# Kernel tuning notes

Measured on AMD Instinct MI355X. Metric: run time of the kernel, lower is better.

Reference implementation:

```python
import jax, jax.numpy as jnp
import numpy as np
import jax.scipy.linalg as jsl

# ---- module constants (mirror __init__ buffers) ----
T0, T1, DT = 0.0, 1.0, 1e-3
DIM, NSTEPS, M, TQ, B = 8, 2048, 64, 1024, 1
DS = (T1 - T0) / NSTEPS
STEPS = jnp.linspace(T0, T1, NSTEPS + 1)            # [S+1]
ZPTS = jnp.linspace(T0 + DT * 5.5, T1 - DT * 5.5, M)  # inducing points [M]
SQRT_DS = float(np.sqrt(DS))
SQRT_DT = float(np.sqrt(DT))


def _hurst(t, y0, W1, b1, W2, b2, Wc1, bc1, Wc2, bc2, dw, cw):
    # compute_hurst: sigmoid(driving_action(t)*dw + condition_net(y0)*cw)
    tc_in = t.reshape(-1, 1)                                             # [N,1]
    feat = jnp.concatenate([jnp.sin(tc_in), jnp.cos(tc_in), tc_in], -1)  # [N,3]
    tc = jax.nn.sigmoid(jnp.tanh(feat @ W1.T + b1) @ W2.T + b2)          # [N,dim]
    pc = jax.nn.sigmoid(jnp.tanh(y0 @ Wc1.T + bc1) @ Wc2.T + bc2)        # [1,dim]
    return jax.nn.sigmoid(tc * dw + pc * cw)                             # [N,dim]


def _safe_pow(x, a):
    # x**a for x>=0, with well-defined (zero) gradient at x==0
    mask = x > 0
    xs = jnp.where(mask, x, 1.0)
    return jnp.where(mask, xs ** a, 0.0)


def _compute_weight(t, y0, params, eps=1e-12):
    # compute_weight (Muniandy et al. weight); returns [S, N, dim]
    h = _hurst(t, y0, *params)[None]                              # [1,N,dim]
    d0 = jax.nn.relu(t[None, :] - STEPS[:-1, None])[..., None]    # [S,N,1]
    d1 = jax.nn.relu(t[None, :] - STEPS[1:, None])[..., None]     # [S,N,1]
    w = jnp.sqrt(_safe_pow(d0, 2.0 * h) - _safe_pow(d1, 2.0 * h) + eps)
    w = w / jnp.sqrt(2.0 * h * DS)
    return w / jnp.exp(jax.lax.lgamma(h + 0.5))


def _increment_weight(t, y0, params):
    # increment_weight: g_i / dt (finite difference of clamped weights)
    wa = jnp.maximum(_compute_weight(t, y0, params), 0.0)
    wb = jnp.maximum(_compute_weight(t + DT, y0, params), 0.0)
    return jnp.maximum((wb - wa) * SQRT_DS / DT, 0.0)             # [S,N,dim]


def _forward(t, y0, eps_z, W1, b1, W2, b2, Wc1, bc1, Wc2, bc2, dw, cw):
    params = (W1, b1, W2, b2, Wc1, bc1, Wc2, bc2, dw, cw)
    # --- precompute (inducing points) ---
    Kz = _increment_weight(ZPTS, y0, params)                # [S,M,dim]
    Kzz = jnp.einsum('smd,skd->dmk', Kz, Kz)                # [dim,M,M]
    Lz = jnp.linalg.cholesky(Kzz + 1e-6 * jnp.eye(M, dtype=Kzz.dtype))
    delta_Bz = jnp.einsum('dmk,dkb->dmb', Lz, eps_z)        # [dim,M,B]
    # --- forward (mean / sqrt(var)*sqrt(dt)) ---
    Kt = _increment_weight(t, y0, params)                   # [S,T,dim]
    Ktz = jnp.einsum('std,smd->dtm', Kt, Kz)                # [dim,T,M]
    alpha = jax.vmap(lambda L, b: jsl.cho_solve((L, True), b))(
        Lz, jnp.swapaxes(Ktz, -1, -2))                      # [dim,M,T]
    mean = jnp.einsum('dmt,dmb->dtb', alpha, delta_Bz)      # [dim,T,B]
    Ktt = jnp.einsum('std,sud->dtu', Kt, Kt)                # [dim,T,T]
    var = Ktt - jnp.einsum('dmt,dmu->dtu', alpha, alpha)    # [dim,T,T]
    std = jnp.sqrt(jnp.maximum(var, 1e-12)) * SQRT_DT
    return mean.reshape(-1, DIM), std.reshape(-1, DIM)


def setup_inputs() -> dict:
    key = jax.random.key(0)
    ks = jax.random.split(key, 12)
    return {
        't': jax.random.uniform(ks[0], (TQ,), jnp.float32, T0 + 0.05, T1 - 0.05),
        'y0': jax.random.normal(ks[1], (1, 1), jnp.float32),
        'eps_z': jax.random.normal(ks[2], (DIM, M, B), jnp.float32),
        'W1': jax.random.normal(ks[3], (10, 3), jnp.float32) * 0.3,
        'b1': jax.random.normal(ks[4], (10,), jnp.float32) * 0.1,
        'W2': jax.random.normal(ks[5], (DIM, 10), jnp.float32) * 0.3,
        'b2': jax.random.normal(ks[6], (DIM,), jnp.float32) * 0.1,
        'Wc1': jax.random.normal(ks[7], (10, 1), jnp.float32) * 0.3,
        'bc1': jax.random.normal(ks[8], (10,), jnp.float32) * 0.1,
        'Wc2': jax.random.normal(ks[9], (DIM, 10), jnp.float32) * 0.3,
        'bc2': jax.random.normal(ks[10], (DIM,), jnp.float32) * 0.1,
        'dw': jnp.array([0.5], jnp.float32),
        'cw': jnp.array([0.5], jnp.float32),
    }


def reference(t, y0, eps_z, W1, b1, W2, b2, Wc1, bc1, Wc2, bc2, dw, cw):
    return _forward(t, y0, eps_z, W1, b1, W2, b2, Wc1, bc1, Wc2, bc2, dw, cw)
```

## Files before the change

### kernel.cpp

```cpp
#include <hip/hip_runtime.h>
#include <cmath>

#define DIMN 8
#define SSTEPS 2048
#define MZ 64
#define TQN 1024
#define DS_F    4.8828125e-4f
#define DT_F    1.0e-3f
#define SCALE_F 22.09708691207961f
#define SQRTDT_F 0.031622776601683794f
#define LN2_F   0.6931471805599453f

typedef _Float16 f16x8 __attribute__((ext_vector_type(8)));
typedef float f32x4 __attribute__((ext_vector_type(4)));

__device__ __forceinline__ float sigmoidf_(float x) { return 1.f / (1.f + expf(-x)); }

__device__ __forceinline__ void gl_lds16(const _Float16* g, _Float16* l)
{
    __builtin_amdgcn_global_load_lds(
        (const __attribute__((address_space(1))) unsigned int*)g,
        (__attribute__((address_space(3))) unsigned int*)l, 16, 0, 0);
}

__global__ void coef_kernel(const float* __restrict__ t_in, const float* __restrict__ y0,
                            const float* __restrict__ W1, const float* __restrict__ b1,
                            const float* __restrict__ W2, const float* __restrict__ b2,
                            const float* __restrict__ Wc1, const float* __restrict__ bc1,
                            const float* __restrict__ Wc2, const float* __restrict__ bc2,
                            const float* __restrict__ dw, const float* __restrict__ cw,
                            float4* __restrict__ coef_t, float4* __restrict__ coef_z,
                            float* __restrict__ times_z)
{
    int gid = blockIdx.x * blockDim.x + threadIdx.x;
    if (gid >= TQN + MZ) return;
    bool isz = gid >= TQN;
    float tv;
    if (!isz) {
        tv = t_in[gid];
    } else {
        int j = gid - TQN;
        tv = 0.0055f + (float)j * (0.989f / 63.0f);
        times_z[j] = tv;
    }
    float y = y0[0];
    float hc[10];
    #pragma unroll
    for (int j = 0; j < 10; ++j) hc[j] = tanhf(y * Wc1[j] + bc1[j]);
    float pc[DIMN];
    #pragma unroll
    for (int d = 0; d < DIMN; ++d) {
        float s = bc2[d];
        #pragma unroll
        for (int j = 0; j < 10; ++j) s += hc[j] * Wc2[d * 10 + j];
        pc[d] = sigmoidf_(s);
    }
    float dww = dw[0], cww = cw[0];
    float4 outv[DIMN];
    for (int which = 0; which < 2; ++which) {
        float tt = (which == 0) ? tv : tv + DT_F;
        float st = sinf(tt), ct = cosf(tt);
        float hid[10];
        #pragma unroll
        for (int j = 0; j < 10; ++j)
            hid[j] = tanhf(st * W1[j * 3 + 0] + ct * W1[j * 3 + 1] + tt * W1[j * 3 + 2] + b1[j]);
        #pragma unroll
        for (int d = 0; d < DIMN; ++d) {
            float s = b2[d];
            #pragma unroll
            for (int j = 0; j < 10; ++j) s += hid[j] * W2[d * 10 + j];
            float tc = sigmoidf_(s);
            float h = sigmoidf_(tc * dww + pc[d] * cww);
            float e = 2.f * h;
            float c = rsqrtf(e * DS_F) / tgammaf(h + 0.5f);
            if (which == 0) { outv[d].x = e; outv[d].y = c; }
            else            { outv[d].z = e; outv[d].w = c; }
        }
    }
    float4* dst = isz ? (coef_z + (size_t)(gid - TQN) * DIMN) : (coef_t + (size_t)gid * DIMN);
    #pragma unroll
    for (int d = 0; d < DIMN; ++d) dst[d] = outv[d];
}

__device__ __forceinline__ void side_weights(float tt, float e, float c, int sbase,
                                             float (&w)[8])
{
    float xprev = tt - (float)sbase * DS_F;
    float pa = 0.f;
    if (xprev > 0.f) pa = __builtin_amdgcn_exp2f(e * __builtin_amdgcn_logf(xprev));
    #pragma unroll
    for (int k = 1; k <= 8; ++k) {
        float xk = tt - (float)(sbase + k) * DS_F;
        float D, pan;
        if (xk > 0.f) {
            float om = xk * __builtin_amdgcn_rcpf(xprev);
            float y2 = e * __builtin_amdgcn_logf(om);
            float wl = y2 * LN2_F;
            float em = wl * (1.f + wl * (0.5f + wl * (0.16666667f + wl * (0.041666668f + wl * 0.008333334f))));
            float g = -em;
            if (wl < -0.3f) g = 1.f - __builtin_amdgcn_exp2f(y2);
            D = pa * g;
            pan = pa - D;
        } else {
            D = pa;
            pan = 0.f;
        }
        w[k - 1] = __builtin_amdgcn_sqrtf(D + 1e-12f) * c;
        pa = pan;
        xprev = xk;
    }
}

__device__ __forceinline__ unsigned pack_hl(float v)
{
    _Float16 h = (_Float16)v;
    _Float16 l = (_Float16)(v - (float)h);
    unsigned short hu = __builtin_bit_cast(unsigned short, h);
    unsigned short lu = __builtin_bit_cast(unsigned short, l);
    return (unsigned)hu | ((unsigned)lu << 16);
}

__global__ __launch_bounds__(256) void kmat_t_kernel(const float* __restrict__ times,
                                                     const float4* __restrict__ coef,
                                                     _Float16* __restrict__ KThi,
                                                     _Float16* __restrict__ KTlo)
{
    int tid = threadIdx.x;
    int txx = tid & 31, sidx = tid >> 5;
    int t = blockIdx.x * 32 + txx;
    int sbase = blockIdx.y * 64 + sidx * 8;
    int d = blockIdx.z;
    __shared__ unsigned shhl[32][65];
    float tq = times[t];
    float4 cf = coef[(size_t)t * DIMN + d];
    float wa[8], wb[8];
    side_weights(tq,        cf.x, cf.y, sbase, wa);
    side_weights(tq + DT_F, cf.z, cf.w, sbase, wb);
    #pragma unroll
    for (int k = 0; k < 8; ++k) {
        float v = fmaxf(wb[k] - wa[k], 0.f) * SCALE_F;
        shhl[txx][sidx * 8 + k] = pack_hl(v);
    }
    __syncthreads();
    int tl = tid >> 3, sc = tid & 7;
    unsigned dwv[8];
    #pragma unroll
    for (int j = 0; j < 8; ++j) dwv[j] = shhl[tl][sc * 8 + j];
    uint4 hv, lv;
    hv.x = __builtin_amdgcn_perm(dwv[1], dwv[0], 0x05040100u);
    hv.y = __builtin_amdgcn_perm(dwv[3], dwv[2], 0x05040100u);
    hv.z = __builtin_amdgcn_perm(dwv[5], dwv[4], 0x05040100u);
    hv.w = __builtin_amdgcn_perm(dwv[7], dwv[6], 0x05040100u);
    lv.x = __builtin_amdgcn_perm(dwv[1], dwv[0], 0x07060302u);
    lv.y = __builtin_amdgcn_perm(dwv[3], dwv[2], 0x07060302u);
    lv.z = __builtin_amdgcn_perm(dwv[5], dwv[4], 0x07060302u);
    lv.w = __builtin_amdgcn_perm(dwv[7], dwv[6], 0x07060302u);
    size_t o = ((size_t)(d * 1024) + blockIdx.x * 32 + tl) * 2048 + blockIdx.y * 64 + sc * 8;
    *(uint4*)&KThi[o] = hv;
    *(uint4*)&KTlo[o] = lv;
}

__global__ __launch_bounds__(256) void kmat_z_kernel(const float* __restrict__ times,
                                                     const float4* __restrict__ coef,
                                                     float* __restrict__ Kz,
                                                     _Float16* __restrict__ KzThi,
                                                     _Float16* __restrict__ KzTlo)
{
    int tid = threadIdx.x;
    int txx = tid & 31, sidx = tid >> 5;
    int m = blockIdx.x * 32 + txx;
    int sbase = blockIdx.y * 64 + sidx * 8;
    int d = blockIdx.z;
    __shared__ unsigned shhl[32][65];
    float tq = times[m];
    float4 cf = coef[(size_t)m * DIMN + d];
    float wa[8], wb[8];
    side_weights(tq,        cf.x, cf.y, sbase, wa);
    side_weights(tq + DT_F, cf.z, cf.w, sbase, wb);
    #pragma unroll
    for (int k = 0; k < 8; ++k) {
        float v = fmaxf(wb[k] - wa[k], 0.f) * SCALE_F;
        Kz[((size_t)d * SSTEPS + sbase + k) * 64 + m] = v;
        shhl[txx][sidx * 8 + k] = pack_hl(v);
    }
    __syncthreads();
    int tl = tid >> 3, sc = tid & 7;
    unsigned dwv[8];
    #pragma unroll
    for (int j = 0; j < 8; ++j) dwv[j] = shhl[tl][sc * 8 + j];
    uint4 hv, lv;
    hv.x = __builtin_amdgcn_perm(dwv[1], dwv[0], 0x05040100u);
    hv.y = __builtin_amdgcn_perm(dwv[3], dwv[2], 0x05040100u);
    hv.z = __builtin_amdgcn_perm(dwv[5], dwv[4], 0x05040100u);
    hv.w = __builtin_amdgcn_perm(dwv[7], dwv[6], 0x05040100u);
    lv.x = __builtin_amdgcn_perm(dwv[1], dwv[0], 0x07060302u);
    lv.y = __builtin_amdgcn_perm(dwv[3], dwv[2], 0x07060302u);
    lv.z = __builtin_amdgcn_perm(dwv[5], dwv[4], 0x07060302u);
    lv.w = __builtin_amdgcn_perm(dwv[7], dwv[6], 0x07060302u);
    size_t o = ((size_t)(d * 64) + blockIdx.x * 32 + tl) * 2048 + blockIdx.y * 64 + sc * 8;
    *(uint4*)&KzThi[o] = hv;
    *(uint4*)&KzTlo[o] = lv;
}

__global__ __launch_bounds__(256) void kzz_partial_kernel(const float* __restrict__ Kz,
                                                          float* __restrict__ part)
{
    int kidx = blockIdx.x;
    int d = blockIdx.y;
    int tid = threadIdx.x, tx = tid & 15, ty = tid >> 4;
    __shared__ float As[32][64];
    float acc[4][4] = {};
    const float* base = Kz + ((size_t)d * SSTEPS + (size_t)kidx * 256) * 64;
    for (int c = 0; c < 8; ++c) {
        __syncthreads();
        #pragma unroll
        for (int l = 0; l < 2; ++l) {
            int idx = tid + l * 256;
            int r = idx >> 4, c4 = idx & 15;
            *(float4*)&As[r][c4 * 4] = *(const float4*)(base + (size_t)(c * 32 + r) * 64 + c4 * 4);
        }
        __syncthreads();
        #pragma unroll
        for (int k = 0; k < 32; ++k) {
            float av[4], bv[4];
            *(float4*)&av[0] = *(float4*)&As[k][ty * 4];
            *(float4*)&bv[0] = *(float4*)&As[k][tx * 4];
            #pragma unroll
            for (int i = 0; i < 4; ++i)
                #pragma unroll
                for (int j = 0; j < 4; ++j) acc[i][j] += av[i] * bv[j];
        }
    }
    float* dst = part + (size_t)(kidx * DIMN + d) * 4096;
    #pragma unroll
    for (int i = 0; i < 4; ++i)
        *(float4*)&dst[(size_t)(ty * 4 + i) * 64 + tx * 4] =
            make_float4(acc[i][0], acc[i][1], acc[i][2], acc[i][3]);
}

__global__ void reduce_kernel(const float* __restrict__ in, float* __restrict__ out,
                              int n, int parts)
{
    int i = blockIdx.x * 256 + threadIdx.x;
    if (i >= n) return;
    float s = 0.f;
    for (int p = 0; p < parts; ++p) s += in[(size_t)p * n + i];
    out[i] = s;
}

__global__ __launch_bounds__(64) void chol_kernel(const float* __restrict__ Kzz,
                                                  const float* __restrict__ eps_z,
                                                  float* __restrict__ Lz, float* __restrict__ dBz)
{
    int d = blockIdx.x, i = threadIdx.x;
    __shared__ float A[64][65];
    for (int r = 0; r < 64; ++r)
        A[r][i] = Kzz[(size_t)d * 4096 + (size_t)r * 64 + i] + ((r == i) ? 1e-6f : 0.f);
    __syncthreads();
    for (int j = 0; j < 64; ++j) {
        float s = 0.f;
        if (i >= j) {
            s = A[i][j];
            for (int k = 0; k < j; ++k) s -= A[i][k] * A[j][k];
        }
        __syncthreads();
        if (i == j) A[j][j] = sqrtf(fmaxf(s, 1e-30f));
        __syncthreads();
        if (i > j) A[i][j] = s / A[j][j];
        __syncthreads();
    }
    for (int r = 0; r < 64; ++r)
        Lz[(size_t)d * 4096 + (size_t)r * 64 + i] = (i <= r) ? A[r][i] : 0.f;
    float s = 0.f;
    for (int k = 0; k <= i; ++k) s += A[i][k] * eps_z[d * 64 + k];
    dBz[d * 64 + i] = s;
}

__global__ __launch_bounds__(256, 2) void ktz_mfma_kernel(const _Float16* __restrict__ KThi,
                                                          const _Float16* __restrict__ KTlo,
                                                          const _Float16* __restrict__ KzThi,
                                                          const _Float16* __restrict__ KzTlo,
                                                          float* __restrict__ part)
{
    int tid = threadIdx.x;
    int wave = tid >> 6, lane = tid & 63;
    int n = lane & 15, q = lane >> 4;
    int lr = lane >> 2, lc = (lane & 3) * 8;
    int d = blockIdx.x;
    int t0 = blockIdx.y * 128;
    int split = blockIdx.z;
    int wr = (wave >> 1) * 64, wc = (wave & 1) * 32;

    __shared__ _Float16 Ah[2][128][32], Al[2][128][32];
    __shared__ _Float16 Bh[2][64][32],  Bl[2][64][32];

    f32x4 acc[4][2];
    #pragma unroll
    for (int i = 0; i < 4; ++i)
        #pragma unroll
        for (int j = 0; j < 2; ++j) acc[i][j] = (f32x4)0.f;

    const size_t aRow = (size_t)(d * 1024 + t0);
    const size_t bRow = (size_t)(d * 64);
    int segA = wave * 32;
    int segB = wave * 16;

    auto stage = [&](int buf, int c) {
        int s0 = split * 512 + c * 32;
        size_t ga = (aRow + segA + lr) * 2048 + s0 + lc;
        size_t gb = (bRow + segB + lr) * 2048 + s0 + lc;
        gl_lds16(KThi + ga,               &Ah[buf][segA][0]);
        gl_lds16(KThi + ga + 16 * 2048,   &Ah[buf][segA + 16][0]);
        gl_lds16(KTlo + ga,               &Al[buf][segA][0]);
        gl_lds16(KTlo + ga + 16 * 2048,   &Al[buf][segA + 16][0]);
        gl_lds16(KzThi + gb,              &Bh[buf][segB][0]);
        gl_lds16(KzTlo + gb,              &Bl[buf][segB][0]);
    };

    stage(0, 0);
    __syncthreads();
    for (int c = 0; c < 16; ++c) {
        int buf = c & 1;
        if (c + 1 < 16) stage(buf ^ 1, c + 1);
        f16x8 fAh[4], fAl[4], fBh[2], fBl[2];
        #pragma unroll
        for (int i = 0; i < 4; ++i) {
            fAh[i] = *(f16x8*)&Ah[buf][wr + i * 16 + n][q * 8];
            fAl[i] = *(f16x8*)&Al[buf][wr + i * 16 + n][q * 8];
        }
        #pragma unroll
        for (int j = 0; j < 2; ++j) {
            fBh[j] = *(f16x8*)&Bh[buf][wc + j * 16 + n][q * 8];
            fBl[j] = *(f16x8*)&Bl[buf][wc + j * 16 + n][q * 8];
        }
        #pragma unroll
        for (int i = 0; i < 4; ++i)
            #pragma unroll
            for (int j = 0; j < 2; ++j) {
                acc[i][j] = __builtin_amdgcn_mfma_f32_16x16x32_f16(fAh[i], fBh[j], acc[i][j], 0, 0, 0);
                acc[i][j] = __builtin_amdgcn_mfma_f32_16x16x32_f16(fAh[i], fBl[j], acc[i][j], 0, 0, 0);
                acc[i][j] = __builtin_amdgcn_mfma_f32_16x16x32_f16(fAl[i], fBh[j], acc[i][j], 0, 0, 0);
            }
        __syncthreads();
    }
    float* dst = part + ((size_t)(split * DIMN + d)) * 1024 * 64;
    #pragma unroll
    for (int i = 0; i < 4; ++i)
        #pragma unroll
        for (int j = 0; j < 2; ++j)
            #pragma unroll
            for (int r = 0; r < 4; ++r) {
                int t = t0 + wr + i * 16 + q * 4 + r;
                dst[(size_t)t * 64 + wc + j * 16 + n] = acc[i][j][r];
            }
}

__global__ __launch_bounds__(64) void solve_kernel(const float* __restrict__ Lz,
                                                   const float* __restrict__ part2,
                                                   const float* __restrict__ dBz,
                                                   _Float16* __restrict__ aPhi,
                                                   _Float16* __restrict__ aPlo,
                                                   _Float16* __restrict__ aNhi,
                                                   _Float16* __restrict__ aNlo,
                                                   float* __restrict__ out0)
{
    int d = blockIdx.y;
    int t0 = blockIdx.x * 64;
    int i = threadIdx.x;
    __shared__ float L[64][65];
    __shared__ float bL[64][65];
    __shared__ float inv[64];
    __shared__ float dB[64];
    for (int r = 0; r < 64; ++r)
        L[r][i] = Lz[(size_t)d * 4096 + (size_t)r * 64 + i];
    dB[i] = dBz[d * 64 + i];
    for (int r = 0; r < 64; ++r) {
        size_t base = ((size_t)d * 1024 + t0 + r) * 64 + i;
        float s = part2[base] + part2[base + 524288] + part2[base + 1048576] + part2[base + 1572864];
        bL[i][r] = s;
    }
    __syncthreads();
    inv[i] = 1.f / L[i][i];
    __syncthreads();
    for (int j = 0; j < 64; ++j) {
        float s = bL[j][i];
        for (int k = 0; k < j; ++k) s -= L[j][k] * bL[k][i];
        bL[j][i] = s * inv[j];
    }
    for (int j = 63; j >= 0; --j) {
        float s = bL[j][i];
        for (int k = j + 1; k < 64; ++k) s -= L[k][j] * bL[k][i];
        bL[j][i] = s * inv[j];
    }
    float mn = 0.f;
    for (int m = 0; m < 64; ++m) mn += bL[m][i] * dB[m];
    out0[d * 1024 + t0 + i] = mn;
    size_t o = ((size_t)(d * 1024 + t0 + i)) * 64;
    for (int g = 0; g < 8; ++g) {
        union { _Float16 h[8]; float4 v; } ph, pl, nh, nl;
        #pragma unroll
        for (int k = 0; k < 8; ++k) {
            float x = bL[g * 8 + k][i];
            _Float16 h = (_Float16)x;
            _Float16 lo = (_Float16)(x - (float)h);
            ph.h[k] = h;  pl.h[k] = lo;
            nh.h[k] = -h; nl.h[k] = -lo;
        }
        *(float4*)&aPhi[o + g * 8] = ph.v;
        *(float4*)&aPlo[o + g * 8] = pl.v;
        *(float4*)&aNhi[o + g * 8] = nh.v;
        *(float4*)&aNlo[o + g * 8] = nl.v;
    }
}

__global__ __launch_bounds__(128, 2) void var_mfma_kernel(const _Float16* __restrict__ KThi,
                                                          const _Float16* __restrict__ KTlo,
                                                          const _Float16* __restrict__ aPhi,
                                                          const _Float16* __restrict__ aPlo,
                                                          const _Float16* __restrict__ aNhi,
                                                          const _Float16* __restrict__ aNlo,
                                                          float* __restrict__ out1)
{
    int tid = threadIdx.x;
    int wave = tid >> 6, lane = tid & 63;
    int n = lane & 15, q = lane >> 4;
    int lr = lane >> 2;
    int lcs = (((lane & 3) ^ ((lr >> 1) & 3)) * 8);
    int qs  = ((q ^ ((n >> 1) & 3)) * 8);
    int d = blockIdx.x;
    int ti = 0, rem = blockIdx.y;
    while (rem >= 16 - 2 * ti) { rem -= 16 - 2 * ti; ++ti; }
    int uj = 2 * ti + rem;
    int t0 = ti * 128, u0 = uj * 64;
    int wr = wave * 64;

    __shared__ _Float16 Ah[2][128][32], Al[2][128][32];
    __shared__ _Float16 Bh[2][64][32],  Bl[2][64][32];

    f32x4 acc[4][4];
    #pragma unroll
    for (int i = 0; i < 4; ++i)
        #pragma unroll
        for (int j = 0; j < 4; ++j) acc[i][j] = (f32x4)0.f;

    const size_t aRow = (size_t)(d * 1024 + t0);
    const size_t bRow = (size_t)(d * 1024 + u0);
    int segA = wave * 64;
    int segB = wave * 32;

    auto stage = [&](int buf, int ck) {
        const _Float16 *ph, *pl, *qh, *ql;
        size_t str; int col;
        if (ck < 64) { ph = KThi; pl = KTlo; qh = KThi; ql = KTlo; str = 2048; col = ck * 32; }
        else         { ph = aPhi; pl = aPlo; qh = aNhi; ql = aNlo; str = 64;  col = (ck - 64) * 32; }
        size_t ga = (aRow + segA + lr) * str + col + lcs;
        size_t gb = (bRow + segB + lr) * str + col + lcs;
        gl_lds16(ph + ga,            &Ah[buf][segA][0]);
        gl_lds16(ph + ga + 16 * str, &Ah[buf][segA + 16][0]);
        gl_lds16(ph + ga + 32 * str, &Ah[buf][segA + 32][0]);
        gl_lds16(ph + ga + 48 * str, &Ah[buf][segA + 48][0]);
        gl_lds16(pl + ga,            &Al[buf][segA][0]);
        gl_lds16(pl + ga + 16 * str, &Al[buf][segA + 16][0]);
        gl_lds16(pl + ga + 32 * str, &Al[buf][segA + 32][0]);
        gl_lds16(pl + ga + 48 * str, &Al[buf][segA + 48][0]);
        gl_lds16(qh + gb,            &Bh[buf][segB][0]);
        gl_lds16(qh + gb + 16 * str, &Bh[buf][segB + 16][0]);
        gl_lds16(ql + gb,            &Bl[buf][segB][0]);
        gl_lds16(ql + gb + 16 * str, &Bl[buf][segB + 16][0]);
    };

    stage(0, 0);
    __syncthreads();
    for (int ck = 0; ck < 66; ++ck) {
        int buf = ck & 1;
        if (ck + 1 < 66) stage(buf ^ 1, ck + 1);
        f16x8 fAh[4], fAl[4], fBh[4], fBl[4];
        #pragma unroll
        for (int i = 0; i < 4; ++i) {
            fAh[i] = *(f16x8*)&Ah[buf][wr + i * 16 + n][qs];
            fAl[i] = *(f16x8*)&Al[buf][wr + i * 16 + n][qs];
            fBh[i] = *(f16x8*)&Bh[buf][i * 16 + n][qs];
            fBl[i] = *(f16x8*)&Bl[buf][i * 16 + n][qs];
        }
        #pragma unroll
        for (int i = 0; i < 4; ++i)
            #pragma unroll
            for (int j = 0; j < 4; ++j) {
                acc[i][j] = __builtin_amdgcn_mfma_f32_16x16x32_f16(fAh[i], fBh[j], acc[i][j], 0, 0, 0);
                acc[i][j] = __builtin_amdgcn_mfma_f32_16x16x32_f16(fAh[i], fBl[j], acc[i][j], 0, 0, 0);
                acc[i][j] = __builtin_amdgcn_mfma_f32_16x16x32_f16(fAl[i], fBh[j], acc[i][j], 0, 0, 0);
            }
        __syncthreads();
    }
    float* dst = out1 + ((size_t)d << 20);
    int tw0 = t0 + wr;
    bool above = (u0 >= tw0 + 64);
    bool below = (u0 + 64 <= tw0);
    if (!below) {
        #pragma unroll
        for (int i = 0; i < 4; ++i) {
            int tb = tw0 + i * 16 + q * 4;
            #pragma unroll
            for (int j = 0; j < 4; ++j) {
                int u = u0 + j * 16 + n;
                float fv[4];
                #pragma unroll
                for (int r = 0; r < 4; ++r)
                    fv[r] = sqrtf(fmaxf(acc[i][j][r], 1e-12f)) * SQRTDT_F;
                if (above) {
                    #pragma unroll
                    for (int r = 0; r < 4; ++r)
                        dst[(size_t)(tb + r) * 1024 + u] = fv[r];
                    *(float4*)&dst[(size_t)u * 1024 + tb] = make_float4(fv[0], fv[1], fv[2], fv[3]);
                } else {
                    #pragma unroll
                    for (int r = 0; r < 4; ++r) {
                        int t = tb + r;
                        if (u >= t) dst[(size_t)t * 1024 + u] = fv[r];
                        if (u > t)  dst[(size_t)u * 1024 + t] = fv[r];
                    }
                }
            }
        }
    }
}

extern "C" void kernel_launch(void* const* d_in, const int* in_sizes, int n_in,
                              void* d_out, int out_size, void* d_ws, size_t ws_size,
                              hipStream_t stream)
{
    const float* t_in  = (const float*)d_in[0];
    const float* y0    = (const float*)d_in[1];
    const float* eps_z = (const float*)d_in[2];
    const float* W1    = (const float*)d_in[3];
    const float* b1    = (const float*)d_in[4];
    const float* W2    = (const float*)d_in[5];
    const float* b2    = (const float*)d_in[6];
    const float* Wc1   = (const float*)d_in[7];
    const float* bc1   = (const float*)d_in[8];
    const float* Wc2   = (const float*)d_in[9];
    const float* bc2   = (const float*)d_in[10];
    const float* dw    = (const float*)d_in[11];
    const float* cw    = (const float*)d_in[12];

    float* ws = (float*)d_ws;
    size_t off = 0;
    auto carve = [&](size_t n) { float* p = ws + off; off += n; return p; };
    float* coef_t   = carve(32768);
    float* coef_z   = carve(2048);
    float* times_z  = carve(64);
    float* Kzz      = carve(32768);
    float* Lz       = carve(32768);
    float* dBz      = carve(512);
    float* Kz       = carve(1048576);
    _Float16* KThi  = (_Float16*)carve(8388608);
    _Float16* KTlo  = (_Float16*)carve(8388608);
    _Float16* KzThi = (_Float16*)carve(524288);
    _Float16* KzTlo = (_Float16*)carve(524288);
    float* part1    = carve(262144);
    float* part2    = carve(2097152);
    _Float16* aPhi  = (_Float16*)carve(262144);
    _Float16* aPlo  = (_Float16*)carve(262144);
    _Float16* aNhi  = (_Float16*)carve(262144);
    _Float16* aNlo  = (_Float16*)carve(262144);

    float* out0 = (float*)d_out;
    float* out1 = out0 + (size_t)DIMN * 1024;

    coef_kernel<<<9, 128, 0, stream>>>(t_in, y0, W1, b1, W2, b2, Wc1, bc1, Wc2, bc2, dw, cw,
                                       (float4*)coef_t, (float4*)coef_z, times_z);
    kmat_t_kernel<<<dim3(32, 32, 8), 256, 0, stream>>>(t_in, (const float4*)coef_t,
                                                       KThi, KTlo);
    kmat_z_kernel<<<dim3(2, 32, 8), 256, 0, stream>>>(times_z, (const float4*)coef_z,
                                                      Kz, KzThi, KzTlo);
    kzz_partial_kernel<<<dim3(8, 8), 256, 0, stream>>>(Kz, part1);
    reduce_kernel<<<128, 256, 0, stream>>>(part1, Kzz, 32768, 8);
    chol_kernel<<<8, 64, 0, stream>>>(Kzz, eps_z, Lz, dBz);
    ktz_mfma_kernel<<<dim3(8, 8, 4), 256, 0, stream>>>(KThi, KTlo, KzThi, KzTlo, part2);
    solve_kernel<<<dim3(16, 8), 64, 0, stream>>>(Lz, part2, dBz, aPhi, aPlo, aNhi, aNlo, out0);
    var_mfma_kernel<<<dim3(8, 72), 128, 0, stream>>>(KThi, KTlo, aPhi, aPlo, aNhi, aNlo, out1);
}
```

Measured before the change: 389.0 us.

## Use four waves per var tile with 2x2 wave grid and deeper async LDS pipeline

The variance MFMA kernel now runs 256 threads per block, with each wave computing a 64x32 sub-tile instead of 64x64. The per-wave accumulator and register footprint shrink, and occupancy rises under the new launch bounds. Loads are prefetched two chunks ahead with explicit vmcnt/lgkmcnt waits and raw s_barriers in place of __syncthreads. The staging for a buffer is issued only after all waves have read that buffer into registers. MFMA sections also raise wave priority. This should hide global-to-LDS latency better, at the cost of fragile hand-counted waitcnt values and more LDS read traffic per MFMA.

```diff
diff --git a/kernel.cpp b/kernel.cpp
--- a/kernel.cpp
+++ b/kernel.cpp
@@ -413,7 +413,7 @@
     }
 }
 
-__global__ __launch_bounds__(128, 2) void var_mfma_kernel(const _Float16* __restrict__ KThi,
+__global__ __launch_bounds__(256, 3) void var_mfma_kernel(const _Float16* __restrict__ KThi,
                                                           const _Float16* __restrict__ KTlo,
                                                           const _Float16* __restrict__ aPhi,
                                                           const _Float16* __restrict__ aPlo,
@@ -432,77 +432,84 @@
     while (rem >= 16 - 2 * ti) { rem -= 16 - 2 * ti; ++ti; }
     int uj = 2 * ti + rem;
     int t0 = ti * 128, u0 = uj * 64;
-    int wr = wave * 64;
+    int wr = (wave >> 1) * 64, wc = (wave & 1) * 32;
 
     __shared__ _Float16 Ah[2][128][32], Al[2][128][32];
     __shared__ _Float16 Bh[2][64][32],  Bl[2][64][32];
 
-    f32x4 acc[4][4];
+    f32x4 acc[4][2];
     #pragma unroll
     for (int i = 0; i < 4; ++i)
         #pragma unroll
-        for (int j = 0; j < 4; ++j) acc[i][j] = (f32x4)0.f;
+        for (int j = 0; j < 2; ++j) acc[i][j] = (f32x4)0.f;
 
     const size_t aRow = (size_t)(d * 1024 + t0);
     const size_t bRow = (size_t)(d * 1024 + u0);
-    int segA = wave * 64;
-    int segB = wave * 32;
+    int sa = wave * 32;
+    int sb = wave * 16;
 
     auto stage = [&](int buf, int ck) {
         const _Float16 *ph, *pl, *qh, *ql;
         size_t str; int col;
         if (ck < 64) { ph = KThi; pl = KTlo; qh = KThi; ql = KTlo; str = 2048; col = ck * 32; }
         else         { ph = aPhi; pl = aPlo; qh = aNhi; ql = aNlo; str = 64;  col = (ck - 64) * 32; }
-        size_t ga = (aRow + segA + lr) * str + col + lcs;
-        size_t gb = (bRow + segB + lr) * str + col + lcs;
-        gl_lds16(ph + ga,            &Ah[buf][segA][0]);
-        gl_lds16(ph + ga + 16 * str, &Ah[buf][segA + 16][0]);
-        gl_lds16(ph + ga + 32 * str, &Ah[buf][segA + 32][0]);
-        gl_lds16(ph + ga + 48 * str, &Ah[buf][segA + 48][0]);
-        gl_lds16(pl + ga,            &Al[buf][segA][0]);
-        gl_lds16(pl + ga + 16 * str, &Al[buf][segA + 16][0]);
-        gl_lds16(pl + ga + 32 * str, &Al[buf][segA + 32][0]);
-        gl_lds16(pl + ga + 48 * str, &Al[buf][segA + 48][0]);
-        gl_lds16(qh + gb,            &Bh[buf][segB][0]);
-        gl_lds16(qh + gb + 16 * str, &Bh[buf][segB + 16][0]);
-        gl_lds16(ql + gb,            &Bl[buf][segB][0]);
-        gl_lds16(ql + gb + 16 * str, &Bl[buf][segB + 16][0]);
+        size_t ga = (aRow + sa + lr) * str + col + lcs;
+        size_t gb = (bRow + sb + lr) * str + col + lcs;
+        gl_lds16(ph + ga,            &Ah[buf][sa][0]);
+        gl_lds16(ph + ga + 16 * str, &Ah[buf][sa + 16][0]);
+        gl_lds16(pl + ga,            &Al[buf][sa][0]);
+        gl_lds16(pl + ga + 16 * str, &Al[buf][sa + 16][0]);
+        gl_lds16(qh + gb,            &Bh[buf][sb][0]);
+        gl_lds16(ql + gb,            &Bl[buf][sb][0]);
     };
 
     stage(0, 0);
-    __syncthreads();
+    stage(1, 1);
     for (int ck = 0; ck < 66; ++ck) {
         int buf = ck & 1;
-        if (ck + 1 < 66) stage(buf ^ 1, ck + 1);
-        f16x8 fAh[4], fAl[4], fBh[4], fBl[4];
+        if (ck < 65) asm volatile("s_waitcnt vmcnt(6)" ::: "memory");
+        else         asm volatile("s_waitcnt vmcnt(0)" ::: "memory");
+        __builtin_amdgcn_s_barrier();
+        __builtin_amdgcn_sched_barrier(0);
+        f16x8 fAh[4], fAl[4], fBh[2], fBl[2];
         #pragma unroll
         for (int i = 0; i < 4; ++i) {
             fAh[i] = *(f16x8*)&Ah[buf][wr + i * 16 + n][qs];
             fAl[i] = *(f16x8*)&Al[buf][wr + i * 16 + n][qs];
-            fBh[i] = *(f16x8*)&Bh[buf][i * 16 + n][qs];
-            fBl[i] = *(f16x8*)&Bl[buf][i * 16 + n][qs];
-        }
+        }
+        #pragma unroll
+        for (int j = 0; j < 2; ++j) {
+            fBh[j] = *(f16x8*)&Bh[buf][wc + j * 16 + n][qs];
+            fBl[j] = *(f16x8*)&Bl[buf][wc + j * 16 + n][qs];
+        }
+        asm volatile("s_waitcnt lgkmcnt(0)" ::: "memory");
+        __builtin_amdgcn_sched_barrier(0);
+        __builtin_amdgcn_s_barrier();
+        __builtin_amdgcn_sched_barrier(0);
+        if (ck + 2 < 66) stage(buf, ck + 2);
+        __builtin_amdgcn_s_setprio(1);
         #pragma unroll
         for (int i = 0; i < 4; ++i)
             #pragma unroll
-            for (int j = 0; j < 4; ++j) {
+            for (int j = 0; j < 2; ++j) {
                 acc[i][j] = __builtin_amdgcn_mfma_f32_16x16x32_f16(fAh[i], fBh[j], acc[i][j], 0, 0, 0);
                 acc[i][j] = __builtin_amdgcn_mfma_f32_16x16x32_f16(fAh[i], fBl[j], acc[i][j], 0, 0, 0);
                 acc[i][j] = __builtin_amdgcn_mfma_f32_16x16x32_f16(fAl[i], fBh[j], acc[i][j], 0, 0, 0);
             }
-        __syncthreads();
+        __builtin_amdgcn_s_setprio(0);
     }
     float* dst = out1 + ((size_t)d << 20);
     int tw0 = t0 + wr;
-    bool above = (u0 >= tw0 + 64);
-    bool below = (u0 + 64 <= tw0);
+    int uw0 = u0 + wc;
+    bool above = (uw0 >= tw0 + 64);
+    bool below = (uw0 + 32 <= tw0);
     if (!below) {
         #pragma unroll
         for (int i = 0; i < 4; ++i) {
             int tb = tw0 + i * 16 + q * 4;
             #pragma unroll
-            for (int j = 0; j < 4; ++j) {
-                int u = u0 + j * 16 + n;
+            for (int j = 0; j < 2; ++j) {
+                int u = uw0 + j * 16 + n;
                 float fv[4];
                 #pragma unroll
                 for (int r = 0; r < 4; ++r)
@@ -578,5 +585,5 @@
     chol_kernel<<<8, 64, 0, stream>>>(Kzz, eps_z, Lz, dBz);
     ktz_mfma_kernel<<<dim3(8, 8, 4), 256, 0, stream>>>(KThi, KTlo, KzThi, KzTlo, part2);
     solve_kernel<<<dim3(16, 8), 64, 0, stream>>>(Lz, part2, dBz, aPhi, aPlo, aNhi, aNlo, out0);
-    var_mfma_kernel<<<dim3(8, 72), 128, 0, stream>>>(KThi, KTlo, aPhi, aPlo, aNhi, aNlo, out1);
-}
+    var_mfma_kernel<<<dim3(8, 72), 256, 0, stream>>>(KThi, KTlo, aPhi, aPlo, aNhi, aNlo, out1);
+}
```

Result: faster. 367.4 us (-5.6%).

## Retile variance GEMM to single-wave 64x64 tiles and tighten ktz pipeline sync

Applied to the files above, without the earlier changes.

The variance MFMA kernel now launches one wave per block with a 64x64 tile over the triangular (t,u) grid, 136 blocks per dim instead of 72. The diagonal is covered exactly, with no tiles that are partly below it, and block-wide barriers are replaced by explicit vmcnt/lgkmcnt waits. The ktz kernel moves its barrier to the top of each iteration behind a vmcnt(0) wait and raises wave priority around the MFMA block. The aim is to use more CUs and cut barrier overhead. In exchange, each block does less data reuse per tile and the hand-written waitcnt scheme could be fragile.

```diff
diff --git a/kernel.cpp b/kernel.cpp
--- a/kernel.cpp
+++ b/kernel.cpp
@@ -318,9 +318,11 @@
     };
 
     stage(0, 0);
-    __syncthreads();
     for (int c = 0; c < 16; ++c) {
         int buf = c & 1;
+        asm volatile("s_waitcnt vmcnt(0)" ::: "memory");
+        __builtin_amdgcn_s_barrier();
+        __builtin_amdgcn_sched_barrier(0);
         if (c + 1 < 16) stage(buf ^ 1, c + 1);
         f16x8 fAh[4], fAl[4], fBh[2], fBl[2];
         #pragma unroll
@@ -333,6 +335,7 @@
             fBh[j] = *(f16x8*)&Bh[buf][wc + j * 16 + n][q * 8];
             fBl[j] = *(f16x8*)&Bl[buf][wc + j * 16 + n][q * 8];
         }
+        __builtin_amdgcn_s_setprio(1);
         #pragma unroll
         for (int i = 0; i < 4; ++i)
             #pragma unroll
@@ -341,7 +344,7 @@
                 acc[i][j] = __builtin_amdgcn_mfma_f32_16x16x32_f16(fAh[i], fBl[j], acc[i][j], 0, 0, 0);
                 acc[i][j] = __builtin_amdgcn_mfma_f32_16x16x32_f16(fAl[i], fBh[j], acc[i][j], 0, 0, 0);
             }
-        __syncthreads();
+        __builtin_amdgcn_s_setprio(0);
     }
     float* dst = part + ((size_t)(split * DIMN + d)) * 1024 * 64;
     #pragma unroll
@@ -413,29 +416,27 @@
     }
 }
 
-__global__ __launch_bounds__(128, 2) void var_mfma_kernel(const _Float16* __restrict__ KThi,
-                                                          const _Float16* __restrict__ KTlo,
-                                                          const _Float16* __restrict__ aPhi,
-                                                          const _Float16* __restrict__ aPlo,
-                                                          const _Float16* __restrict__ aNhi,
-                                                          const _Float16* __restrict__ aNlo,
-                                                          float* __restrict__ out1)
-{
-    int tid = threadIdx.x;
-    int wave = tid >> 6, lane = tid & 63;
+__global__ __launch_bounds__(64) void var_mfma_kernel(const _Float16* __restrict__ KThi,
+                                                      const _Float16* __restrict__ KTlo,
+                                                      const _Float16* __restrict__ aPhi,
+                                                      const _Float16* __restrict__ aPlo,
+                                                      const _Float16* __restrict__ aNhi,
+                                                      const _Float16* __restrict__ aNlo,
+                                                      float* __restrict__ out1)
+{
+    int lane = threadIdx.x;
     int n = lane & 15, q = lane >> 4;
     int lr = lane >> 2;
     int lcs = (((lane & 3) ^ ((lr >> 1) & 3)) * 8);
     int qs  = ((q ^ ((n >> 1) & 3)) * 8);
     int d = blockIdx.x;
     int ti = 0, rem = blockIdx.y;
-    while (rem >= 16 - 2 * ti) { rem -= 16 - 2 * ti; ++ti; }
-    int uj = 2 * ti + rem;
-    int t0 = ti * 128, u0 = uj * 64;
-    int wr = wave * 64;
-
-    __shared__ _Float16 Ah[2][128][32], Al[2][128][32];
-    __shared__ _Float16 Bh[2][64][32],  Bl[2][64][32];
+    while (rem >= 16 - ti) { rem -= 16 - ti; ++ti; }
+    int uj = ti + rem;
+    int t0 = ti * 64, u0 = uj * 64;
+
+    __shared__ _Float16 Ah[2][64][32], Al[2][64][32];
+    __shared__ _Float16 Bh[2][64][32], Bl[2][64][32];
 
     f32x4 acc[4][4];
     #pragma unroll
@@ -445,40 +446,38 @@
 
     const size_t aRow = (size_t)(d * 1024 + t0);
     const size_t bRow = (size_t)(d * 1024 + u0);
-    int segA = wave * 64;
-    int segB = wave * 32;
 
     auto stage = [&](int buf, int ck) {
         const _Float16 *ph, *pl, *qh, *ql;
         size_t str; int col;
         if (ck < 64) { ph = KThi; pl = KTlo; qh = KThi; ql = KTlo; str = 2048; col = ck * 32; }
         else         { ph = aPhi; pl = aPlo; qh = aNhi; ql = aNlo; str = 64;  col = (ck - 64) * 32; }
-        size_t ga = (aRow + segA + lr) * str + col + lcs;
-        size_t gb = (bRow + segB + lr) * str + col + lcs;
-        gl_lds16(ph + ga,            &Ah[buf][segA][0]);
-        gl_lds16(ph + ga + 16 * str, &Ah[buf][segA + 16][0]);
-        gl_lds16(ph + ga + 32 * str, &Ah[buf][segA + 32][0]);
-        gl_lds16(ph + ga + 48 * str, &Ah[buf][segA + 48][0]);
-        gl_lds16(pl + ga,            &Al[buf][segA][0]);
-        gl_lds16(pl + ga + 16 * str, &Al[buf][segA + 16][0]);
-        gl_lds16(pl + ga + 32 * str, &Al[buf][segA + 32][0]);
-        gl_lds16(pl + ga + 48 * str, &Al[buf][segA + 48][0]);
-        gl_lds16(qh + gb,            &Bh[buf][segB][0]);
-        gl_lds16(qh + gb + 16 * str, &Bh[buf][segB + 16][0]);
-        gl_lds16(ql + gb,            &Bl[buf][segB][0]);
-        gl_lds16(ql + gb + 16 * str, &Bl[buf][segB + 16][0]);
+        size_t ga = (aRow + lr) * str + col + lcs;
+        size_t gb = (bRow + lr) * str + col + lcs;
+        #pragma unroll
+        for (int rr = 0; rr < 64; rr += 16) {
+            gl_lds16(ph + ga + (size_t)rr * str, &Ah[buf][rr][0]);
+            gl_lds16(pl + ga + (size_t)rr * str, &Al[buf][rr][0]);
+            gl_lds16(qh + gb + (size_t)rr * str, &Bh[buf][rr][0]);
+            gl_lds16(ql + gb + (size_t)rr * str, &Bl[buf][rr][0]);
+        }
     };
 
     stage(0, 0);
-    __syncthreads();
     for (int ck = 0; ck < 66; ++ck) {
         int buf = ck & 1;
-        if (ck + 1 < 66) stage(buf ^ 1, ck + 1);
+        if (ck + 1 < 66) {
+            asm volatile("s_waitcnt lgkmcnt(0)" ::: "memory");
+            stage(buf ^ 1, ck + 1);
+            asm volatile("s_waitcnt vmcnt(16)" ::: "memory");
+        } else {
+            asm volatile("s_waitcnt vmcnt(0)" ::: "memory");
+        }
         f16x8 fAh[4], fAl[4], fBh[4], fBl[4];
         #pragma unroll
         for (int i = 0; i < 4; ++i) {
-            fAh[i] = *(f16x8*)&Ah[buf][wr + i * 16 + n][qs];
-            fAl[i] = *(f16x8*)&Al[buf][wr + i * 16 + n][qs];
+            fAh[i] = *(f16x8*)&Ah[buf][i * 16 + n][qs];
+            fAl[i] = *(f16x8*)&Al[buf][i * 16 + n][qs];
             fBh[i] = *(f16x8*)&Bh[buf][i * 16 + n][qs];
             fBl[i] = *(f16x8*)&Bl[buf][i * 16 + n][qs];
         }
@@ -490,35 +489,30 @@
                 acc[i][j] = __builtin_amdgcn_mfma_f32_16x16x32_f16(fAh[i], fBl[j], acc[i][j], 0, 0, 0);
                 acc[i][j] = __builtin_amdgcn_mfma_f32_16x16x32_f16(fAl[i], fBh[j], acc[i][j], 0, 0, 0);
             }
-        __syncthreads();
     }
     float* dst = out1 + ((size_t)d << 20);
-    int tw0 = t0 + wr;
-    bool above = (u0 >= tw0 + 64);
-    bool below = (u0 + 64 <= tw0);
-    if (!below) {
-        #pragma unroll
-        for (int i = 0; i < 4; ++i) {
-            int tb = tw0 + i * 16 + q * 4;
+    bool above = (uj > ti);
+    #pragma unroll
+    for (int i = 0; i < 4; ++i) {
+        int tb = t0 + i * 16 + q * 4;
+        #pragma unroll
+        for (int j = 0; j < 4; ++j) {
+            int u = u0 + j * 16 + n;
+            float fv[4];
             #pragma unroll
-            for (int j = 0; j < 4; ++j) {
-                int u = u0 + j * 16 + n;
-                float fv[4];
+            for (int r = 0; r < 4; ++r)
+                fv[r] = sqrtf(fmaxf(acc[i][j][r], 1e-12f)) * SQRTDT_F;
+            if (above) {
                 #pragma unroll
                 for (int r = 0; r < 4; ++r)
-                    fv[r] = sqrtf(fmaxf(acc[i][j][r], 1e-12f)) * SQRTDT_F;
-                if (above) {
-                    #pragma unroll
-                    for (int r = 0; r < 4; ++r)
-                        dst[(size_t)(tb + r) * 1024 + u] = fv[r];
-                    *(float4*)&dst[(size_t)u * 1024 + tb] = make_float4(fv[0], fv[1], fv[2], fv[3]);
-                } else {
-                    #pragma unroll
-                    for (int r = 0; r < 4; ++r) {
-                        int t = tb + r;
-                        if (u >= t) dst[(size_t)t * 1024 + u] = fv[r];
-                        if (u > t)  dst[(size_t)u * 1024 + t] = fv[r];
-                    }
+                    dst[(size_t)(tb + r) * 1024 + u] = fv[r];
+                *(float4*)&dst[(size_t)u * 1024 + tb] = make_float4(fv[0], fv[1], fv[2], fv[3]);
+            } else {
+                #pragma unroll
+                for (int r = 0; r < 4; ++r) {
+                    int t = tb + r;
+                    if (u >= t) dst[(size_t)t * 1024 + u] = fv[r];
+                    if (u > t)  dst[(size_t)u * 1024 + t] = fv[r];
                 }
             }
         }
@@ -578,5 +572,5 @@
     chol_kernel<<<8, 64, 0, stream>>>(Kzz, eps_z, Lz, dBz);
     ktz_mfma_kernel<<<dim3(8, 8, 4), 256, 0, stream>>>(KThi, KTlo, KzThi, KzTlo, part2);
     solve_kernel<<<dim3(16, 8), 64, 0, stream>>>(Lz, part2, dBz, aPhi, aPlo, aNhi, aNlo, out0);
-    var_mfma_kernel<<<dim3(8, 72), 128, 0, stream>>>(KThi, KTlo, aPhi, aPlo, aNhi, aNlo, out1);
-}
+    var_mfma_kernel<<<dim3(8, 136), 64, 0, stream>>>(KThi, KTlo, aPhi, aPlo, aNhi, aNlo, out1);
+}
```

Measured after the change: 421.2 us. +8.3%, slower.
